# Kernel tuning notes

Measured on AMD Instinct MI355X. Metric: run time of the kernel, lower is better.

The kernel has to match this reference:

```python
import jax, jax.numpy as jnp
import numpy as np

N = 8192
F_IN = 256
F_OUT = 128
ALPHA = 0.2  # leaky relu negative slope


def _leaky(x):
    return jnp.where(x >= 0, x, ALPHA * x)


def setup_inputs() -> dict:
    key = jax.random.key(0)
    ks = jax.random.split(key, 12)
    nodes = jax.random.normal(ks[0], (N, F_IN), dtype=jnp.float32)
    adj = (jax.random.uniform(ks[1], (N, N)) < 0.05).astype(jnp.float32)
    adj = jnp.maximum(adj, jnp.eye(N, dtype=jnp.float32))
    s = 0.02
    W1 = jax.random.normal(ks[2], (F_IN, F_OUT), dtype=jnp.float32) * s
    b1 = jnp.zeros((F_OUT,), jnp.float32)
    W2 = jax.random.normal(ks[3], (F_OUT, F_OUT), dtype=jnp.float32) * s
    b2 = jnp.zeros((F_OUT,), jnp.float32)
    W3 = jax.random.normal(ks[4], (F_OUT, F_OUT), dtype=jnp.float32) * s
    b3 = jnp.zeros((F_OUT,), jnp.float32)
    W4 = jax.random.normal(ks[5], (F_OUT, F_OUT), dtype=jnp.float32) * s
    b4 = jnp.zeros((F_OUT,), jnp.float32)
    a_w = jax.random.normal(ks[6], (2 * F_OUT,), dtype=jnp.float32) * s
    a_b = jnp.zeros((), jnp.float32)
    return {"nodes": nodes, "adj": adj, "W1": W1, "b1": b1, "W2": W2, "b2": b2,
            "W3": W3, "b3": b3, "W4": W4, "b4": b4, "a_w": a_w, "a_b": a_b}


def reference(nodes, adj, W1, b1, W2, b2, W3, b3, W4, b4, a_w, a_b):
    # 4-layer linear stack
    h = jax.nn.relu(nodes @ W1 + b1)
    h = jax.nn.relu(h @ W2 + b2)
    h = jax.nn.relu(h @ W3 + b3)
    h = h @ W4 + b4  # (N, F_OUT)
    # a([h_i, h_j]) is linear -> split into src/dst components instead of
    # materializing the (N, N, 2F) repeat+cat tensor; identical math.
    a1, a2 = a_w[:F_OUT], a_w[F_OUT:]
    s_src = h @ a1  # (N,)
    s_dst = h @ a2  # (N,)
    e = _leaky(s_src[:, None] + s_dst[None, :] + a_b)  # (N, N)
    e = jnp.where(adj >= 0.5, e, -jnp.inf)
    attention = jax.nn.softmax(e, axis=1)
    # dropout is identity in eval mode
    return _leaky(attention @ h)  # (N, F_OUT)
```

## Files before the change

kernel.cpp:

```cpp
#include <hip/hip_runtime.h>
#include <hip/hip_bf16.h>

#define N_NODES 8192
#define F_IN    256
#define F_OUT   128
#define CAP     1024

typedef float f4v __attribute__((ext_vector_type(4)));

__device__ __forceinline__ float leaky(float x) { return x >= 0.f ? x : 0.2f * x; }

__global__ __launch_bounds__(256) void mlp_fused(
    const float* __restrict__ nodes,
    const float* __restrict__ W1, const float* __restrict__ b1,
    const float* __restrict__ W2, const float* __restrict__ b2,
    const float* __restrict__ W3, const float* __restrict__ b3,
    const float* __restrict__ W4, const float* __restrict__ b4,
    const float* __restrict__ aw,
    float* __restrict__ h_out, float* __restrict__ ss, float* __restrict__ sd) {
  __shared__ float As[32][36];
  __shared__ float Ws[32][128];
  __shared__ float hTa[128][36];
  __shared__ float hTb[128][36];
  __shared__ float awS[2 * F_OUT];
  __shared__ float sred[2][8][32];

  const int tid = threadIdx.x;
  const int bm0 = blockIdx.x * 32;
  const int mt = tid >> 5;
  const int nt = tid & 31;
  const int ar = tid >> 3;
  const int ac = tid & 7;

  awS[tid] = aw[tid];

  float acc[4][4] = {};

  for (int k0 = 0; k0 < F_IN; k0 += 32) {
    const float4 av = *(const float4*)(nodes + (size_t)(bm0 + ar) * F_IN + k0 + ac * 4);
    float4 wv[4];
#pragma unroll
    for (int i = 0; i < 4; ++i) {
      const int kk = i * 8 + (tid >> 5);
      wv[i] = *(const float4*)(W1 + (size_t)(k0 + kk) * F_OUT + nt * 4);
    }
    __syncthreads();
    As[ac * 4 + 0][ar] = av.x;
    As[ac * 4 + 1][ar] = av.y;
    As[ac * 4 + 2][ar] = av.z;
    As[ac * 4 + 3][ar] = av.w;
#pragma unroll
    for (int i = 0; i < 4; ++i) {
      const int kk = i * 8 + (tid >> 5);
      *(float4*)&Ws[kk][nt * 4] = wv[i];
    }
    __syncthreads();
#pragma unroll
    for (int k = 0; k < 32; ++k) {
      const float4 a = *(const float4*)&As[k][mt * 4];
      const float4 w = *(const float4*)&Ws[k][nt * 4];
      acc[0][0] += a.x * w.x; acc[0][1] += a.x * w.y; acc[0][2] += a.x * w.z; acc[0][3] += a.x * w.w;
      acc[1][0] += a.y * w.x; acc[1][1] += a.y * w.y; acc[1][2] += a.y * w.z; acc[1][3] += a.y * w.w;
      acc[2][0] += a.z * w.x; acc[2][1] += a.z * w.y; acc[2][2] += a.z * w.z; acc[2][3] += a.z * w.w;
      acc[3][0] += a.w * w.x; acc[3][1] += a.w * w.y; acc[3][2] += a.w * w.z; acc[3][3] += a.w * w.w;
    }
  }
  {
    const float4 bv = *(const float4*)(b1 + nt * 4);
#pragma unroll
    for (int i = 0; i < 4; ++i) {
      hTa[nt * 4 + 0][mt * 4 + i] = fmaxf(acc[i][0] + bv.x, 0.f);
      hTa[nt * 4 + 1][mt * 4 + i] = fmaxf(acc[i][1] + bv.y, 0.f);
      hTa[nt * 4 + 2][mt * 4 + i] = fmaxf(acc[i][2] + bv.z, 0.f);
      hTa[nt * 4 + 3][mt * 4 + i] = fmaxf(acc[i][3] + bv.w, 0.f);
    }
  }

  const float* Wl[3] = {W2, W3, W4};
  const float* bl[3] = {b2, b3, b4};
  float* hin = &hTa[0][0];
  float* hout = &hTb[0][0];
  for (int l = 0; l < 3; ++l) {
#pragma unroll
    for (int i = 0; i < 4; ++i)
#pragma unroll
      for (int j = 0; j < 4; ++j) acc[i][j] = 0.f;
    for (int k0 = 0; k0 < F_OUT; k0 += 32) {
      float4 wv[4];
#pragma unroll
      for (int i = 0; i < 4; ++i) {
        const int kk = i * 8 + (tid >> 5);
        wv[i] = *(const float4*)(Wl[l] + (size_t)(k0 + kk) * F_OUT + nt * 4);
      }
      __syncthreads();
#pragma unroll
      for (int i = 0; i < 4; ++i) {
        const int kk = i * 8 + (tid >> 5);
        *(float4*)&Ws[kk][nt * 4] = wv[i];
      }
      __syncthreads();
#pragma unroll
      for (int k = 0; k < 32; ++k) {
        const float4 a = *(const float4*)(hin + (size_t)(k0 + k) * 36 + mt * 4);
        const float4 w = *(const float4*)&Ws[k][nt * 4];
        acc[0][0] += a.x * w.x; acc[0][1] += a.x * w.y; acc[0][2] += a.x * w.z; acc[0][3] += a.x * w.w;
        acc[1][0] += a.y * w.x; acc[1][1] += a.y * w.y; acc[1][2] += a.y * w.z; acc[1][3] += a.y * w.w;
        acc[2][0] += a.z * w.x; acc[2][1] += a.z * w.y; acc[2][2] += a.z * w.z; acc[2][3] += a.z * w.w;
        acc[3][0] += a.w * w.x; acc[3][1] += a.w * w.y; acc[3][2] += a.w * w.z; acc[3][3] += a.w * w.w;
      }
    }
    const float4 bv = *(const float4*)(bl[l] + nt * 4);
    const bool relu = (l < 2);
#pragma unroll
    for (int i = 0; i < 4; ++i) {
      float o0 = acc[i][0] + bv.x, o1 = acc[i][1] + bv.y;
      float o2 = acc[i][2] + bv.z, o3 = acc[i][3] + bv.w;
      if (relu) {
        o0 = fmaxf(o0, 0.f); o1 = fmaxf(o1, 0.f);
        o2 = fmaxf(o2, 0.f); o3 = fmaxf(o3, 0.f);
      }
      hout[(size_t)(nt * 4 + 0) * 36 + mt * 4 + i] = o0;
      hout[(size_t)(nt * 4 + 1) * 36 + mt * 4 + i] = o1;
      hout[(size_t)(nt * 4 + 2) * 36 + mt * 4 + i] = o2;
      hout[(size_t)(nt * 4 + 3) * 36 + mt * 4 + i] = o3;
    }
    float* t = hin; hin = hout; hout = t;
  }
  __syncthreads();

  {
    const int r = tid & 31;
    const int fg = tid >> 5;
    float s1 = 0.f, s2 = 0.f;
#pragma unroll
    for (int i = 0; i < 16; ++i) {
      const int f = fg * 16 + i;
      const float hv = hin[(size_t)f * 36 + r];
      s1 += hv * awS[f];
      s2 += hv * awS[F_OUT + f];
    }
    sred[0][fg][r] = s1;
    sred[1][fg][r] = s2;
  }
  {
    const int r = tid >> 3;
    const int c = tid & 7;
    float4 o[4];
#pragma unroll
    for (int u = 0; u < 4; ++u) {
      o[u].x = hin[(size_t)(c * 16 + u * 4 + 0) * 36 + r];
      o[u].y = hin[(size_t)(c * 16 + u * 4 + 1) * 36 + r];
      o[u].z = hin[(size_t)(c * 16 + u * 4 + 2) * 36 + r];
      o[u].w = hin[(size_t)(c * 16 + u * 4 + 3) * 36 + r];
    }
    float4* dst = (float4*)(h_out + (size_t)(bm0 + r) * F_OUT + c * 16);
#pragma unroll
    for (int u = 0; u < 4; ++u) dst[u] = o[u];
  }
  __syncthreads();
  if (tid < 32) {
    float s1 = 0.f, s2 = 0.f;
#pragma unroll
    for (int g = 0; g < 8; ++g) { s1 += sred[0][g][tid]; s2 += sred[1][g][tid]; }
    ss[bm0 + tid] = s1;
    sd[bm0 + tid] = s2;
  }
}

__global__ __launch_bounds__(256) void attn_kernel(const float* __restrict__ adj,
                                                   const float* __restrict__ h,
                                                   const float* __restrict__ s_src,
                                                   const float* __restrict__ s_dst,
                                                   const float* __restrict__ ab_ptr,
                                                   float* __restrict__ out) {
  __shared__ float2 pairs[CAP];
  __shared__ float accs[8][32][4];
  __shared__ float red_sum[4];
  __shared__ int cnt;

  const int tid = threadIdx.x;
  const int lane = tid & 63;
  const int wid = tid >> 6;
  const int row = blockIdx.x;
  if (tid == 0) cnt = 0;
  __syncthreads();

  const float sbase = s_src[row] + ab_ptr[0];
  const f4v* arow = (const f4v*)(adj + (size_t)row * N_NODES);
  const float4* dst4 = (const float4*)s_dst;
  const unsigned long long lt = (1ull << lane) - 1ull;

  float lsum = 0.f;
#pragma unroll
  for (int it = 0; it < 8; ++it) {
    const int b4 = it * 256 + tid;
    const f4v av = __builtin_nontemporal_load(arow + b4);
    const float4 sv = dst4[b4];
    const bool hx = av.x >= 0.5f, hy = av.y >= 0.5f, hz = av.z >= 0.5f, hw = av.w >= 0.5f;
    const unsigned long long m0 = __ballot(hx);
    const unsigned long long m1 = __ballot(hy);
    const unsigned long long m2 = __ballot(hz);
    const unsigned long long m3 = __ballot(hw);
    const int t0 = __popcll(m0), t1 = __popcll(m1), t2 = __popcll(m2), t3 = __popcll(m3);
    const int total = t0 + t1 + t2 + t3;
    int wb = 0;
    if (lane == 0) wb = atomicAdd(&cnt, total);
    wb = __shfl(wb, 0, 64);
    const int j0 = b4 * 4;
    if (hx) {
      const int p = wb + __popcll(m0 & lt);
      if (p < CAP) { const float w = __expf(leaky(sbase + sv.x)); pairs[p] = make_float2(w, __int_as_float(j0)); lsum += w; }
    }
    if (hy) {
      const int p = wb + t0 + __popcll(m1 & lt);
      if (p < CAP) { const float w = __expf(leaky(sbase + sv.y)); pairs[p] = make_float2(w, __int_as_float(j0 + 1)); lsum += w; }
    }
    if (hz) {
      const int p = wb + t0 + t1 + __popcll(m2 & lt);
      if (p < CAP) { const float w = __expf(leaky(sbase + sv.z)); pairs[p] = make_float2(w, __int_as_float(j0 + 2)); lsum += w; }
    }
    if (hw) {
      const int p = wb + t0 + t1 + t2 + __popcll(m3 & lt);
      if (p < CAP) { const float w = __expf(leaky(sbase + sv.w)); pairs[p] = make_float2(w, __int_as_float(j0 + 3)); lsum += w; }
    }
  }
#pragma unroll
  for (int o = 1; o < 64; o <<= 1) lsum += __shfl_xor(lsum, o, 64);
  if (lane == 0) red_sum[wid] = lsum;
  __syncthreads();

  const int n = (cnt < CAP) ? cnt : CAP;
  const float inv = 1.f / (red_sum[0] + red_sum[1] + red_sum[2] + red_sum[3]);

  const int g = tid >> 5;
  const int q = tid & 31;
  float4 acc = {0.f, 0.f, 0.f, 0.f};
  const float4* h4 = (const float4*)h;
#pragma unroll 4
  for (int p = g; p < n; p += 8) {
    const float2 pr = pairs[p];
    const float4 hv = h4[(size_t)__float_as_int(pr.y) * 32 + q];
    acc.x += pr.x * hv.x; acc.y += pr.x * hv.y;
    acc.z += pr.x * hv.z; acc.w += pr.x * hv.w;
  }
  *(float4*)&accs[g][q][0] = acc;
  __syncthreads();
  if (tid < 32) {
    float4 t = *(float4*)&accs[0][tid][0];
#pragma unroll
    for (int gg = 1; gg < 8; ++gg) {
      const float4 u = *(float4*)&accs[gg][tid][0];
      t.x += u.x; t.y += u.y; t.z += u.z; t.w += u.w;
    }
    t.x = leaky(t.x * inv); t.y = leaky(t.y * inv);
    t.z = leaky(t.z * inv); t.w = leaky(t.w * inv);
    ((float4*)out)[(size_t)row * 32 + tid] = t;
  }
}

extern "C" void kernel_launch(void* const* d_in, const int* in_sizes, int n_in,
                              void* d_out, int out_size, void* d_ws, size_t ws_size,
                              hipStream_t stream) {
  const float* nodes = (const float*)d_in[0];
  const float* adj   = (const float*)d_in[1];
  const float* W1    = (const float*)d_in[2];
  const float* b1    = (const float*)d_in[3];
  const float* W2    = (const float*)d_in[4];
  const float* b2    = (const float*)d_in[5];
  const float* W3    = (const float*)d_in[6];
  const float* b3    = (const float*)d_in[7];
  const float* W4    = (const float*)d_in[8];
  const float* b4    = (const float*)d_in[9];
  const float* aw    = (const float*)d_in[10];
  const float* ab    = (const float*)d_in[11];
  float* out = (float*)d_out;

  float* h  = (float*)d_ws;
  float* ss = h + (size_t)N_NODES * F_OUT;
  float* sd = ss + N_NODES;

  mlp_fused<<<N_NODES / 32, 256, 0, stream>>>(nodes, W1, b1, W2, b2, W3, b3,
                                              W4, b4, aw, h, ss, sd);
  attn_kernel<<<N_NODES, 256, 0, stream>>>(adj, h, ss, sd, ab, out);
}
```

Measured before the change: 512.9 us.

## Chunk attention rows and overlap adjacency loads with neighbor gather

The attention kernel now handles each row in four column chunks with 512 threads instead of 256. Each chunk is compacted into one of two alternating shared lists and then gathered right away, while the next chunk's adjacency and s_dst values are prefetched in registers. The goal is to hide global load latency behind the h gather instead of running a full compaction pass and then a full gather pass. The costs are one extra barrier per chunk and a per-chunk neighbor cap of 768, which is enough for the ~5% density.

```diff
diff --git a/kernel.cpp b/kernel.cpp
--- a/kernel.cpp
+++ b/kernel.cpp
@@ -4,7 +4,9 @@
 #define N_NODES 8192
 #define F_IN    256
 #define F_OUT   128
-#define CAP     1024
+#define CHUNK   512
+#define NCH     4
+#define CCAP    768
 
 typedef float f4v __attribute__((ext_vector_type(4)));
 
@@ -167,91 +169,100 @@
   }
 }
 
-__global__ __launch_bounds__(256) void attn_kernel(const float* __restrict__ adj,
+__global__ __launch_bounds__(512) void attn_kernel(const float* __restrict__ adj,
                                                    const float* __restrict__ h,
                                                    const float* __restrict__ s_src,
                                                    const float* __restrict__ s_dst,
                                                    const float* __restrict__ ab_ptr,
                                                    float* __restrict__ out) {
-  __shared__ float2 pairs[CAP];
-  __shared__ float accs[8][32][4];
-  __shared__ float red_sum[4];
-  __shared__ int cnt;
+  __shared__ float2 lst[2][CCAP];
+  __shared__ int   cnt[NCH];
+  __shared__ float accs[16][32][4];
+  __shared__ float red_sum[8];
 
   const int tid = threadIdx.x;
   const int lane = tid & 63;
   const int wid = tid >> 6;
   const int row = blockIdx.x;
-  if (tid == 0) cnt = 0;
-  __syncthreads();
+  if (tid < NCH) cnt[tid] = 0;
 
   const float sbase = s_src[row] + ab_ptr[0];
   const f4v* arow = (const f4v*)(adj + (size_t)row * N_NODES);
-  const float4* dst4 = (const float4*)s_dst;
+  const float4* sd4 = (const float4*)s_dst;
+  const float4* h4 = (const float4*)h;
   const unsigned long long lt = (1ull << lane) - 1ull;
+  const int g = tid >> 5;
+  const int q = tid & 31;
+
+  f4v av = __builtin_nontemporal_load(arow + tid);
+  float4 sv = sd4[tid];
 
   float lsum = 0.f;
-#pragma unroll
-  for (int it = 0; it < 8; ++it) {
-    const int b4 = it * 256 + tid;
-    const f4v av = __builtin_nontemporal_load(arow + b4);
-    const float4 sv = dst4[b4];
-    const bool hx = av.x >= 0.5f, hy = av.y >= 0.5f, hz = av.z >= 0.5f, hw = av.w >= 0.5f;
+  float4 acc = {0.f, 0.f, 0.f, 0.f};
+  __syncthreads();
+
+#pragma unroll
+  for (int c = 0; c < NCH; ++c) {
+    const f4v av_c = av;
+    const float4 sv_c = sv;
+    if (c + 1 < NCH) {
+      av = __builtin_nontemporal_load(arow + (c + 1) * CHUNK + tid);
+      sv = sd4[(c + 1) * CHUNK + tid];
+    }
+    const bool hx = av_c.x >= 0.5f, hy = av_c.y >= 0.5f, hz = av_c.z >= 0.5f, hw = av_c.w >= 0.5f;
     const unsigned long long m0 = __ballot(hx);
     const unsigned long long m1 = __ballot(hy);
     const unsigned long long m2 = __ballot(hz);
     const unsigned long long m3 = __ballot(hw);
     const int t0 = __popcll(m0), t1 = __popcll(m1), t2 = __popcll(m2), t3 = __popcll(m3);
-    const int total = t0 + t1 + t2 + t3;
     int wb = 0;
-    if (lane == 0) wb = atomicAdd(&cnt, total);
+    if (lane == 0) wb = atomicAdd(&cnt[c], t0 + t1 + t2 + t3);
     wb = __shfl(wb, 0, 64);
-    const int j0 = b4 * 4;
+    const int j0 = (c * CHUNK + tid) * 4;
+    float2* lc = lst[c & 1];
     if (hx) {
       const int p = wb + __popcll(m0 & lt);
-      if (p < CAP) { const float w = __expf(leaky(sbase + sv.x)); pairs[p] = make_float2(w, __int_as_float(j0)); lsum += w; }
+      if (p < CCAP) { const float w = __expf(leaky(sbase + sv_c.x)); lc[p] = make_float2(w, __int_as_float(j0)); lsum += w; }
     }
     if (hy) {
       const int p = wb + t0 + __popcll(m1 & lt);
-      if (p < CAP) { const float w = __expf(leaky(sbase + sv.y)); pairs[p] = make_float2(w, __int_as_float(j0 + 1)); lsum += w; }
+      if (p < CCAP) { const float w = __expf(leaky(sbase + sv_c.y)); lc[p] = make_float2(w, __int_as_float(j0 + 1)); lsum += w; }
     }
     if (hz) {
       const int p = wb + t0 + t1 + __popcll(m2 & lt);
-      if (p < CAP) { const float w = __expf(leaky(sbase + sv.z)); pairs[p] = make_float2(w, __int_as_float(j0 + 2)); lsum += w; }
+      if (p < CCAP) { const float w = __expf(leaky(sbase + sv_c.z)); lc[p] = make_float2(w, __int_as_float(j0 + 2)); lsum += w; }
     }
     if (hw) {
       const int p = wb + t0 + t1 + t2 + __popcll(m3 & lt);
-      if (p < CAP) { const float w = __expf(leaky(sbase + sv.w)); pairs[p] = make_float2(w, __int_as_float(j0 + 3)); lsum += w; }
-    }
-  }
+      if (p < CCAP) { const float w = __expf(leaky(sbase + sv_c.w)); lc[p] = make_float2(w, __int_as_float(j0 + 3)); lsum += w; }
+    }
+    __syncthreads();
+    const int n = min(cnt[c], CCAP);
+#pragma unroll 2
+    for (int p = g; p < n; p += 16) {
+      const float2 pr = lc[p];
+      const float4 hv = h4[(size_t)__float_as_int(pr.y) * 32 + q];
+      acc.x += pr.x * hv.x; acc.y += pr.x * hv.y;
+      acc.z += pr.x * hv.z; acc.w += pr.x * hv.w;
+    }
+  }
+
 #pragma unroll
   for (int o = 1; o < 64; o <<= 1) lsum += __shfl_xor(lsum, o, 64);
   if (lane == 0) red_sum[wid] = lsum;
-  __syncthreads();
-
-  const int n = (cnt < CAP) ? cnt : CAP;
-  const float inv = 1.f / (red_sum[0] + red_sum[1] + red_sum[2] + red_sum[3]);
-
-  const int g = tid >> 5;
-  const int q = tid & 31;
-  float4 acc = {0.f, 0.f, 0.f, 0.f};
-  const float4* h4 = (const float4*)h;
-#pragma unroll 4
-  for (int p = g; p < n; p += 8) {
-    const float2 pr = pairs[p];
-    const float4 hv = h4[(size_t)__float_as_int(pr.y) * 32 + q];
-    acc.x += pr.x * hv.x; acc.y += pr.x * hv.y;
-    acc.z += pr.x * hv.z; acc.w += pr.x * hv.w;
-  }
   *(float4*)&accs[g][q][0] = acc;
   __syncthreads();
   if (tid < 32) {
     float4 t = *(float4*)&accs[0][tid][0];
 #pragma unroll
-    for (int gg = 1; gg < 8; ++gg) {
+    for (int gg = 1; gg < 16; ++gg) {
       const float4 u = *(float4*)&accs[gg][tid][0];
       t.x += u.x; t.y += u.y; t.z += u.z; t.w += u.w;
     }
+    float s = 0.f;
+#pragma unroll
+    for (int wv = 0; wv < 8; ++wv) s += red_sum[wv];
+    const float inv = 1.f / s;
     t.x = leaky(t.x * inv); t.y = leaky(t.y * inv);
     t.z = leaky(t.z * inv); t.w = leaky(t.w * inv);
     ((float4*)out)[(size_t)row * 32 + tid] = t;
@@ -281,5 +292,5 @@
 
   mlp_fused<<<N_NODES / 32, 256, 0, stream>>>(nodes, W1, b1, W2, b2, W3, b3,
                                               W4, b4, aw, h, ss, sd);
-  attn_kernel<<<N_NODES, 256, 0, stream>>>(adj, h, ss, sd, ab, out);
+  attn_kernel<<<N_NODES, 512, 0, stream>>>(adj, h, ss, sd, ab, out);
 }
```

Result: no change. 513.1 us (+0.0%).

## Tile attention as row-blocked SpMM with shared-memory staged feature chunks

Applied to the files above, without the earlier changes.

Replaces the one-row-per-block attention kernel with blocks of 32 rows that walk the columns in 128-wide chunks. Each chunk of h is staged in shared memory and reused by all 32 rows. Each row builds a small per-chunk neighbor list with atomics and accumulates from LDS, which replaces scattered global gathers of h. The cost is a lot fewer blocks (one per CU), two barriers per chunk with no prefetch of the next chunk, and a per-chunk neighbor cap of 28 that silently drops entries if exceeded.

```diff
diff --git a/kernel.cpp b/kernel.cpp
--- a/kernel.cpp
+++ b/kernel.cpp
@@ -4,9 +4,10 @@
 #define N_NODES 8192
 #define F_IN    256
 #define F_OUT   128
-#define CAP     1024
-
-typedef float f4v __attribute__((ext_vector_type(4)));
+#define RPB     32
+#define CPC     128
+#define NCHK    (N_NODES / CPC)
+#define LCAP    28
 
 __device__ __forceinline__ float leaky(float x) { return x >= 0.f ? x : 0.2f * x; }
 
@@ -167,95 +168,91 @@
   }
 }
 
-__global__ __launch_bounds__(256) void attn_kernel(const float* __restrict__ adj,
-                                                   const float* __restrict__ h,
-                                                   const float* __restrict__ s_src,
-                                                   const float* __restrict__ s_dst,
-                                                   const float* __restrict__ ab_ptr,
-                                                   float* __restrict__ out) {
-  __shared__ float2 pairs[CAP];
-  __shared__ float accs[8][32][4];
-  __shared__ float red_sum[4];
-  __shared__ int cnt;
+__global__ __launch_bounds__(512) void attn_spmm(const float* __restrict__ adj,
+                                                 const float* __restrict__ h,
+                                                 const float* __restrict__ s_src,
+                                                 const float* __restrict__ s_dst,
+                                                 const float* __restrict__ ab_ptr,
+                                                 float* __restrict__ out) {
+  __shared__ float  hS[CPC][128];
+  __shared__ float2 lists[RPB][LCAP];
+  __shared__ int    cnt[2][RPB];
 
   const int tid = threadIdx.x;
-  const int lane = tid & 63;
-  const int wid = tid >> 6;
-  const int row = blockIdx.x;
-  if (tid == 0) cnt = 0;
+  const int r   = tid >> 4;
+  const int k   = tid & 15;
+  const int row = blockIdx.x * RPB + r;
+
+  if (tid < 2 * RPB) ((int*)cnt)[tid] = 0;
+
+  const float sbase = s_src[row] + ab_ptr[0];
+  const float4* h4   = (const float4*)h;
+  const float4* adj4 = (const float4*)(adj + (size_t)row * N_NODES);
+
+  float4 acc0 = {0.f, 0.f, 0.f, 0.f};
+  float4 acc1 = {0.f, 0.f, 0.f, 0.f};
+  float wsum = 0.f;
+
   __syncthreads();
 
-  const float sbase = s_src[row] + ab_ptr[0];
-  const f4v* arow = (const f4v*)(adj + (size_t)row * N_NODES);
-  const float4* dst4 = (const float4*)s_dst;
-  const unsigned long long lt = (1ull << lane) - 1ull;
-
-  float lsum = 0.f;
-#pragma unroll
-  for (int it = 0; it < 8; ++it) {
-    const int b4 = it * 256 + tid;
-    const f4v av = __builtin_nontemporal_load(arow + b4);
-    const float4 sv = dst4[b4];
-    const bool hx = av.x >= 0.5f, hy = av.y >= 0.5f, hz = av.z >= 0.5f, hw = av.w >= 0.5f;
-    const unsigned long long m0 = __ballot(hx);
-    const unsigned long long m1 = __ballot(hy);
-    const unsigned long long m2 = __ballot(hz);
-    const unsigned long long m3 = __ballot(hw);
-    const int t0 = __popcll(m0), t1 = __popcll(m1), t2 = __popcll(m2), t3 = __popcll(m3);
-    const int total = t0 + t1 + t2 + t3;
-    int wb = 0;
-    if (lane == 0) wb = atomicAdd(&cnt, total);
-    wb = __shfl(wb, 0, 64);
-    const int j0 = b4 * 4;
-    if (hx) {
-      const int p = wb + __popcll(m0 & lt);
-      if (p < CAP) { const float w = __expf(leaky(sbase + sv.x)); pairs[p] = make_float2(w, __int_as_float(j0)); lsum += w; }
-    }
-    if (hy) {
-      const int p = wb + t0 + __popcll(m1 & lt);
-      if (p < CAP) { const float w = __expf(leaky(sbase + sv.y)); pairs[p] = make_float2(w, __int_as_float(j0 + 1)); lsum += w; }
-    }
-    if (hz) {
-      const int p = wb + t0 + t1 + __popcll(m2 & lt);
-      if (p < CAP) { const float w = __expf(leaky(sbase + sv.z)); pairs[p] = make_float2(w, __int_as_float(j0 + 2)); lsum += w; }
-    }
-    if (hw) {
-      const int p = wb + t0 + t1 + t2 + __popcll(m3 & lt);
-      if (p < CAP) { const float w = __expf(leaky(sbase + sv.w)); pairs[p] = make_float2(w, __int_as_float(j0 + 3)); lsum += w; }
-    }
-  }
-#pragma unroll
-  for (int o = 1; o < 64; o <<= 1) lsum += __shfl_xor(lsum, o, 64);
-  if (lane == 0) red_sum[wid] = lsum;
-  __syncthreads();
-
-  const int n = (cnt < CAP) ? cnt : CAP;
-  const float inv = 1.f / (red_sum[0] + red_sum[1] + red_sum[2] + red_sum[3]);
-
-  const int g = tid >> 5;
-  const int q = tid & 31;
-  float4 acc = {0.f, 0.f, 0.f, 0.f};
-  const float4* h4 = (const float4*)h;
-#pragma unroll 4
-  for (int p = g; p < n; p += 8) {
-    const float2 pr = pairs[p];
-    const float4 hv = h4[(size_t)__float_as_int(pr.y) * 32 + q];
-    acc.x += pr.x * hv.x; acc.y += pr.x * hv.y;
-    acc.z += pr.x * hv.z; acc.w += pr.x * hv.w;
-  }
-  *(float4*)&accs[g][q][0] = acc;
-  __syncthreads();
-  if (tid < 32) {
-    float4 t = *(float4*)&accs[0][tid][0];
-#pragma unroll
-    for (int gg = 1; gg < 8; ++gg) {
-      const float4 u = *(float4*)&accs[gg][tid][0];
-      t.x += u.x; t.y += u.y; t.z += u.z; t.w += u.w;
-    }
-    t.x = leaky(t.x * inv); t.y = leaky(t.y * inv);
-    t.z = leaky(t.z * inv); t.w = leaky(t.w * inv);
-    ((float4*)out)[(size_t)row * 32 + tid] = t;
-  }
+  for (int c = 0; c < NCHK; ++c) {
+    const int p = c & 1;
+
+    {
+      const size_t base = (size_t)c * CPC * 32;
+#pragma unroll
+      for (int u = 0; u < 8; ++u) {
+        const int idx = u * 512 + tid;
+        ((float4*)hS)[idx] = h4[base + idx];
+      }
+    }
+    {
+      const float4 a0 = adj4[c * 32 + k * 2];
+      const float4 a1 = adj4[c * 32 + k * 2 + 1];
+      const float av[8] = {a0.x, a0.y, a0.z, a0.w, a1.x, a1.y, a1.z, a1.w};
+#pragma unroll
+      for (int e = 0; e < 8; ++e) {
+        if (av[e] >= 0.5f) {
+          const int jl = k * 8 + e;
+          const float w = __expf(leaky(sbase + s_dst[c * CPC + jl]));
+          const int pos = atomicAdd(&cnt[p][r], 1);
+          if (pos < LCAP) {
+            lists[r][pos] = make_float2(w, __int_as_float(jl));
+            wsum += w;
+          }
+        }
+      }
+    }
+    __syncthreads();
+
+    const int n = min(cnt[p][r], LCAP);
+    for (int i = 0; i < n; ++i) {
+      const float2 pr = lists[r][i];
+      const int jl = __float_as_int(pr.y);
+      const float4 b0 = *(const float4*)&hS[jl][k * 4];
+      const float4 b1 = *(const float4*)&hS[jl][64 + k * 4];
+      acc0.x += pr.x * b0.x; acc0.y += pr.x * b0.y;
+      acc0.z += pr.x * b0.z; acc0.w += pr.x * b0.w;
+      acc1.x += pr.x * b1.x; acc1.y += pr.x * b1.y;
+      acc1.z += pr.x * b1.z; acc1.w += pr.x * b1.w;
+    }
+    if (tid < RPB) cnt[1 - p][tid] = 0;
+    __syncthreads();
+  }
+
+  wsum += __shfl_xor(wsum, 1, 64);
+  wsum += __shfl_xor(wsum, 2, 64);
+  wsum += __shfl_xor(wsum, 4, 64);
+  wsum += __shfl_xor(wsum, 8, 64);
+  const float inv = 1.f / wsum;
+
+  float4 o0, o1;
+  o0.x = leaky(acc0.x * inv); o0.y = leaky(acc0.y * inv);
+  o0.z = leaky(acc0.z * inv); o0.w = leaky(acc0.w * inv);
+  o1.x = leaky(acc1.x * inv); o1.y = leaky(acc1.y * inv);
+  o1.z = leaky(acc1.z * inv); o1.w = leaky(acc1.w * inv);
+  ((float4*)out)[(size_t)row * 32 + k]      = o0;
+  ((float4*)out)[(size_t)row * 32 + 16 + k] = o1;
 }
 
 extern "C" void kernel_launch(void* const* d_in, const int* in_sizes, int n_in,
@@ -281,5 +278,5 @@
 
   mlp_fused<<<N_NODES / 32, 256, 0, stream>>>(nodes, W1, b1, W2, b2, W3, b3,
                                               W4, b4, aw, h, ss, sd);
-  attn_kernel<<<N_NODES, 256, 0, stream>>>(adj, h, ss, sd, ab, out);
+  attn_spmm<<<N_NODES / RPB, 512, 0, stream>>>(adj, h, ss, sd, ab, out);
 }
```

Measured after the change: 607.0 us. 18.3% more time.
